# Kernel optimization log

Hardware: AMD Instinct MI355X
Metric: run time of the kernel (lower is better)

## Reference

```python
import jax, jax.numpy as jnp
import numpy as np

_DIMS = [15, 30, 60, 90, 120, 90, 60, 30, 15, 10, 5, 1]


def setup_inputs() -> dict:
    key = jax.random.key(0)
    keys = jax.random.split(key, 1 + 2 * 11)
    inp = {"x": jax.random.normal(keys[0], (524288, 15), dtype=jnp.float32)}
    for i in range(11):
        fan_in, fan_out = _DIMS[i], _DIMS[i + 1]
        bound = 1.0 / np.sqrt(fan_in)
        inp[f"W{i+1}"] = jax.random.uniform(keys[1 + 2 * i], (fan_out, fan_in), minval=-bound, maxval=bound, dtype=jnp.float32)
        inp[f"b{i+1}"] = jax.random.uniform(keys[2 + 2 * i], (fan_out,), minval=-bound, maxval=bound, dtype=jnp.float32)
    return inp


def reference(x, W1, b1, W2, b2, W3, b3, W4, b4, W5, b5, W6, b6, W7, b7, W8, b8, W9, b9, W10, b10, W11, b11):
    Ws = [W1, W2, W3, W4, W5, W6, W7, W8, W9, W10, W11]
    bs = [b1, b2, b3, b4, b5, b6, b7, b8, b9, b10, b11]
    h = x
    # 10 Linear+ReLU layers, funnel 15->30->60->90->120->90->60->30->15->10->5
    for W, b in zip(Ws[:-1], bs[:-1]):
        h = jax.nn.relu(h @ W.T + b)
    # final Linear 5->1 + sigmoid
    return jax.nn.sigmoid(h @ Ws[-1].T + bs[-1])
```

## Files before the change

kernel.cpp:

```cpp
#include <hip/hip_runtime.h>
#include <math.h>


using bf16x8 = __attribute__((ext_vector_type(8))) short;
using f32x4  = __attribute__((ext_vector_type(4))) float;
using u16x8  = __attribute__((ext_vector_type(8))) unsigned short;
using u32x2  = __attribute__((ext_vector_type(2))) unsigned;
typedef __bf16 bf16x2_t __attribute__((ext_vector_type(2)));

namespace {
constexpr int NL = 11;
constexpr int IN_[NL]   = {15, 30, 60, 90, 120, 90, 60, 30, 15, 10, 5};
constexpr int OUT_[NL]  = {30, 60, 90, 120, 90, 60, 30, 15, 10, 5, 1};
constexpr int KP_[NL]   = {32, 32, 64, 96, 128, 96, 64, 32, 32, 32, 32};
constexpr int NP_[NL]   = {32, 64, 96, 128, 96, 64, 32, 16, 16, 16, 16};
constexpr int WOFF_[NL] = {0, 1024, 3072, 9216, 21504, 33792, 39936, 41984, 42496, 43008, 43520};
constexpr int WTOT      = 44032;
constexpr int ACT_OFF   = WTOT;
constexpr int WAVES     = 8;
constexpr int ROWS_PER_BLOCK = WAVES * 32;
constexpr int ARENA     = 4096;
constexpr int LDS_BYTES = (WTOT + WAVES * ARENA) * 2;
}

__device__ __forceinline__ unsigned short f2bf(float f) {
    unsigned u = __float_as_uint(f);
    u += 0x7fffu + ((u >> 16) & 1u);
    return (unsigned short)(u >> 16);
}

__device__ __forceinline__ unsigned pk2(float a, float b) {
#if __has_builtin(__builtin_amdgcn_cvt_pk_bf16_f32)
    return __builtin_bit_cast(unsigned, __builtin_amdgcn_cvt_pk_bf16_f32(a, b));
#else
    bf16x2_t c;
    c[0] = (__bf16)a;
    c[1] = (__bf16)b;
    return __builtin_bit_cast(unsigned, c);
#endif
}

template <int L>
__device__ __forceinline__ void stage_w(const float* __restrict__ W,
                                        const float* __restrict__ B,
                                        short* wlds, int tid) {
    constexpr int KP = KP_[L], NP = NP_[L], INl = IN_[L], OUTl = OUT_[L];
    constexpr int NKT = KP / 32;
    for (int idx = tid; idx < NP * KP; idx += 512) {
        const int f    = idx >> 9;
        const int t    = idx & 511;
        const int quad = t >> 7;
        const int colc = (t >> 3) & 15;
        const int j    = t & 7;
        const int mt   = f / NKT;
        const int kt   = f - mt * NKT;
        const int m    = mt * 16 + colc;
        const int k    = kt * 32 + quad * 8 + j;
        float v = 0.f;
        if (m < OUTl) {
            if (k < INl) v = W[m * INl + k];
            else if (k == INl) v = B[m];
            else if (k == INl + 1) {
                float hf = __builtin_bit_cast(float, (unsigned)f2bf(B[m]) << 16);
                v = B[m] - hf;
            }
        } else if (m == OUTl || m == OUTl + 1) {
            if (k == INl) v = 1.f;
        }
        wlds[WOFF_[L] + idx] = (short)f2bf(v);
    }
}

template <int L>
__device__ __forceinline__ void layer_fwd(const short* __restrict__ wlds,
                                          short* buf, int col, int quad) {
    constexpr int KP   = KP_[L];
    constexpr int NP   = NP_[L];
    constexpr int NKT  = KP / 32;
    constexpr int NMT  = NP / 16;
    constexpr int KPN  = KP_[L + 1];
    constexpr int NKTN = KPN / 32;
    const short* wl = wlds + WOFF_[L];
    const int fo = quad * 128 + col * 8;

    f32x4 acc[NMT][2];
#pragma unroll
    for (int mt = 0; mt < NMT; ++mt)
#pragma unroll
        for (int b = 0; b < 2; ++b)
            acc[mt][b] = f32x4{0.f, 0.f, 0.f, 0.f};

#pragma unroll
    for (int kt = 0; kt < NKT; ++kt) {
        bf16x8 b0 = *(const bf16x8*)(buf + kt * 512 + fo);
        bf16x8 b1 = *(const bf16x8*)(buf + (NKT + kt) * 512 + fo);
#pragma unroll
        for (int mt = 0; mt < NMT; ++mt) {
            bf16x8 af = *(const bf16x8*)(wl + (mt * NKT + kt) * 512 + fo);
            acc[mt][0] = __builtin_amdgcn_mfma_f32_16x16x32_bf16(af, b0, acc[mt][0], 0, 0, 0);
            acc[mt][1] = __builtin_amdgcn_mfma_f32_16x16x32_bf16(af, b1, acc[mt][1], 0, 0, 0);
        }
    }
#pragma unroll
    for (int mt = 0; mt < NMT; ++mt) {
        const int wbase = (mt >> 1) * 512 + ((mt & 1) * 2 + (quad >> 1)) * 128 + col * 8 + (quad & 1) * 4;
#pragma unroll
        for (int b = 0; b < 2; ++b) {
            u32x2 o;
            o[0] = pk2(fmaxf(acc[mt][b][0], 0.f), fmaxf(acc[mt][b][1], 0.f));
            o[1] = pk2(fmaxf(acc[mt][b][2], 0.f), fmaxf(acc[mt][b][3], 0.f));
            *(u32x2*)(buf + b * NKTN * 512 + wbase) = o;
        }
    }
    if constexpr (NP < KPN) {
        u16x8 z = {0, 0, 0, 0, 0, 0, 0, 0};
        if ((quad & 1) == 0) z[0] = (unsigned short)0x3F80;
        *(u16x8*)(buf + (quad >> 1) * NKTN * 512 + (2 + (quad & 1)) * 128 + col * 8) = z;
    }
}

__device__ __forceinline__ void layer_one(bf16x8 af, short* buf, int col, int quad) {
    const int fo = quad * 128 + col * 8;
    bf16x8 b0 = *(const bf16x8*)(buf + fo);
    bf16x8 b1 = *(const bf16x8*)(buf + 512 + fo);
    f32x4 a0 = f32x4{0.f, 0.f, 0.f, 0.f};
    f32x4 a1 = f32x4{0.f, 0.f, 0.f, 0.f};
    a0 = __builtin_amdgcn_mfma_f32_16x16x32_bf16(af, b0, a0, 0, 0, 0);
    a1 = __builtin_amdgcn_mfma_f32_16x16x32_bf16(af, b1, a1, 0, 0, 0);
    const int wbase = (quad >> 1) * 128 + col * 8 + (quad & 1) * 4;
    u32x2 o0, o1;
    o0[0] = pk2(fmaxf(a0[0], 0.f), fmaxf(a0[1], 0.f));
    o0[1] = pk2(fmaxf(a0[2], 0.f), fmaxf(a0[3], 0.f));
    o1[0] = pk2(fmaxf(a1[0], 0.f), fmaxf(a1[1], 0.f));
    o1[1] = pk2(fmaxf(a1[2], 0.f), fmaxf(a1[3], 0.f));
    *(u32x2*)(buf + wbase) = o0;
    *(u32x2*)(buf + 512 + wbase) = o1;
    u16x8 z = {0, 0, 0, 0, 0, 0, 0, 0};
    if ((quad & 1) == 0) z[0] = (unsigned short)0x3F80;
    *(u16x8*)(buf + (quad >> 1) * 512 + (2 + (quad & 1)) * 128 + col * 8) = z;
}

__device__ __forceinline__ float4 ld4(const float* p) {
    float4 t;
    __builtin_memcpy(&t, p, 16);
    return t;
}

__device__ __forceinline__ void fetch_x(const float* __restrict__ x, int row0,
                                        int col, int quad, float4& a0, float4& a1) {
    const float* r0 = x + (long)(row0 + col) * 15;
    const float* r1 = x + (long)(row0 + 16 + col) * 15;
    if (quad < 3) {
        a0 = ld4(r0 + quad * 4);
        a1 = ld4(r1 + quad * 4);
    } else {
        float4 t0 = ld4(r0 + 11), t1 = ld4(r1 + 11);
        a0 = make_float4(t0.y, t0.z, t0.w, 1.f);
        a1 = make_float4(t1.y, t1.z, t1.w, 1.f);
    }
}

__device__ __forceinline__ void stage_x(short* buf, float4 a0, float4 a1,
                                        int col, int quad) {
    const int off = (quad >> 1) * 128 + col * 8 + (quad & 1) * 4;
    u32x2 o0, o1;
    o0[0] = pk2(a0.x, a0.y); o0[1] = pk2(a0.z, a0.w);
    o1[0] = pk2(a1.x, a1.y); o1[1] = pk2(a1.z, a1.w);
    *(u32x2*)(buf + off) = o0;
    *(u32x2*)(buf + 512 + off) = o1;
    u16x8 z = {0, 0, 0, 0, 0, 0, 0, 0};
    if ((quad & 1) == 0) z[0] = (unsigned short)0x3F80;
    *(u16x8*)(buf + (quad >> 1) * 512 + (2 + (quad & 1)) * 128 + col * 8) = z;
}

extern "C" __global__ void __launch_bounds__(512, 2)
mlp_fused(const float* __restrict__ x,
          const float* __restrict__ W0,  const float* __restrict__ B0,
          const float* __restrict__ W1,  const float* __restrict__ B1,
          const float* __restrict__ W2,  const float* __restrict__ B2,
          const float* __restrict__ W3,  const float* __restrict__ B3,
          const float* __restrict__ W4,  const float* __restrict__ B4,
          const float* __restrict__ W5,  const float* __restrict__ B5,
          const float* __restrict__ W6,  const float* __restrict__ B6,
          const float* __restrict__ W7,  const float* __restrict__ B7,
          const float* __restrict__ W8,  const float* __restrict__ B8,
          const float* __restrict__ W9,  const float* __restrict__ B9,
          const float* __restrict__ W10, const float* __restrict__ B10,
          float* __restrict__ out, int nchunks) {
    extern __shared__ short smem[];
    short* wlds = smem;
    short* act  = smem + ACT_OFF;

    const int tid = threadIdx.x;

    stage_w<0>(W0, B0, wlds, tid);
    stage_w<1>(W1, B1, wlds, tid);
    stage_w<2>(W2, B2, wlds, tid);
    stage_w<3>(W3, B3, wlds, tid);
    stage_w<4>(W4, B4, wlds, tid);
    stage_w<5>(W5, B5, wlds, tid);
    stage_w<6>(W6, B6, wlds, tid);
    stage_w<7>(W7, B7, wlds, tid);
    stage_w<8>(W8, B8, wlds, tid);
    stage_w<9>(W9, B9, wlds, tid);
    stage_w<10>(W10, B10, wlds, tid);
    __syncthreads();

    const int wave = tid >> 6;
    const int lane = tid & 63;
    const int col  = lane & 15;
    const int quad = lane >> 4;
    short* buf = act + wave * ARENA;
    const int fo = quad * 128 + col * 8;

    const bf16x8 w7  = *(const bf16x8*)(wlds + WOFF_[7]  + fo);
    const bf16x8 w8  = *(const bf16x8*)(wlds + WOFF_[8]  + fo);
    const bf16x8 w9  = *(const bf16x8*)(wlds + WOFF_[9]  + fo);
    const bf16x8 w10 = *(const bf16x8*)(wlds + WOFF_[10] + fo);

    int chunk = blockIdx.x;
    float4 xa, xb;
    if (chunk < nchunks)
        fetch_x(x, chunk * ROWS_PER_BLOCK + wave * 32, col, quad, xa, xb);

    for (; chunk < nchunks; chunk += gridDim.x) {
        const int row0 = chunk * ROWS_PER_BLOCK + wave * 32;
        stage_x(buf, xa, xb, col, quad);

        const int nxt = chunk + gridDim.x;
        if (nxt < nchunks)
            fetch_x(x, nxt * ROWS_PER_BLOCK + wave * 32, col, quad, xa, xb);

        layer_fwd<0>(wlds, buf, col, quad);
        layer_fwd<1>(wlds, buf, col, quad);
        layer_fwd<2>(wlds, buf, col, quad);
        layer_fwd<3>(wlds, buf, col, quad);
        layer_fwd<4>(wlds, buf, col, quad);
        layer_fwd<5>(wlds, buf, col, quad);
        layer_fwd<6>(wlds, buf, col, quad);
        layer_one(w7, buf, col, quad);
        layer_one(w8, buf, col, quad);
        layer_one(w9, buf, col, quad);

        {
            bf16x8 b0 = *(const bf16x8*)(buf + fo);
            bf16x8 b1 = *(const bf16x8*)(buf + 512 + fo);
            f32x4 a0 = f32x4{0.f, 0.f, 0.f, 0.f};
            f32x4 a1 = f32x4{0.f, 0.f, 0.f, 0.f};
            a0 = __builtin_amdgcn_mfma_f32_16x16x32_bf16(w10, b0, a0, 0, 0, 0);
            a1 = __builtin_amdgcn_mfma_f32_16x16x32_bf16(w10, b1, a1, 0, 0, 0);
            if (quad == 0) {
                out[row0 + col]      = 1.f / (1.f + __expf(-a0[0]));
                out[row0 + 16 + col] = 1.f / (1.f + __expf(-a1[0]));
            }
        }
    }
}

extern "C" void kernel_launch(void* const* d_in, const int* in_sizes, int n_in,
                              void* d_out, int out_size, void* d_ws, size_t ws_size,
                              hipStream_t stream) {
    (void)n_in; (void)d_ws; (void)ws_size; (void)out_size;
    const float* x = (const float*)d_in[0];
    const float* W[11];
    const float* B[11];
    for (int i = 0; i < 11; ++i) {
        W[i] = (const float*)d_in[1 + 2 * i];
        B[i] = (const float*)d_in[2 + 2 * i];
    }
    const int nrows   = in_sizes[0] / 15;
    const int nchunks = nrows / ROWS_PER_BLOCK;

    hipFuncSetAttribute((const void*)mlp_fused,
                        hipFuncAttributeMaxDynamicSharedMemorySize, LDS_BYTES);

    mlp_fused<<<dim3(256), dim3(512), LDS_BYTES, stream>>>(
        x,
        W[0], B[0], W[1], B[1], W[2], B[2], W[3], B[3], W[4], B[4],
        W[5], B[5], W[6], B[6], W[7], B[7], W[8], B[8], W[9], B[9],
        W[10], B[10],
        (float*)d_out, nchunks);
}
```

Measured before the change: 196.8 us.

## Process 64 rows per wave and keep middle-layer activations in registers via shuffles

Each wave now handles 64 rows (four 16-row tiles) instead of 32, so every weight fragment read from LDS feeds four MFMAs instead of two. For layers 2–4 the activations stay in registers: the MFMA output layout is turned into the next layer's B-operand layout with cross-lane shuffles instead of an LDS round trip. The cost is much higher register pressure under launch_bounds(512,2), with possible spills, plus extra shuffle instructions. Per-wave arena usage also grows, and it needs to still fit within ARENA.

```diff
diff --git a/kernel.cpp b/kernel.cpp
--- a/kernel.cpp
+++ b/kernel.cpp
@@ -6,6 +6,7 @@
 using f32x4  = __attribute__((ext_vector_type(4))) float;
 using u16x8  = __attribute__((ext_vector_type(8))) unsigned short;
 using u32x2  = __attribute__((ext_vector_type(2))) unsigned;
+using u32x4  = __attribute__((ext_vector_type(4))) unsigned;
 typedef __bf16 bf16x2_t __attribute__((ext_vector_type(2)));
 
 namespace {
@@ -16,9 +17,8 @@
 constexpr int NP_[NL]   = {32, 64, 96, 128, 96, 64, 32, 16, 16, 16, 16};
 constexpr int WOFF_[NL] = {0, 1024, 3072, 9216, 21504, 33792, 39936, 41984, 42496, 43008, 43520};
 constexpr int WTOT      = 44032;
-constexpr int ACT_OFF   = WTOT;
 constexpr int WAVES     = 8;
-constexpr int ROWS_PER_BLOCK = WAVES * 32;
+constexpr int ROWS_PER_BLOCK = 512;
 constexpr int ARENA     = 4096;
 constexpr int LDS_BYTES = (WTOT + WAVES * ARENA) * 2;
 }
@@ -38,6 +38,30 @@
     c[1] = (__bf16)b;
     return __builtin_bit_cast(unsigned, c);
 #endif
+}
+
+__device__ __forceinline__ u32x2 packrelu(f32x4 a) {
+    u32x2 p;
+    p[0] = pk2(fmaxf(a[0], 0.f), fmaxf(a[1], 0.f));
+    p[1] = pk2(fmaxf(a[2], 0.f), fmaxf(a[3], 0.f));
+    return p;
+}
+
+__device__ __forceinline__ bf16x8 xform(u32x2 pa, u32x2 pb, bool sel, int sA, int sB) {
+    int a0 = __shfl((int)pa[0], sA);
+    int b0 = __shfl((int)pb[0], sA);
+    int a1 = __shfl((int)pa[1], sA);
+    int b1 = __shfl((int)pb[1], sA);
+    int a2 = __shfl((int)pa[0], sB);
+    int b2 = __shfl((int)pb[0], sB);
+    int a3 = __shfl((int)pa[1], sB);
+    int b3 = __shfl((int)pb[1], sB);
+    u32x4 r;
+    r[0] = (unsigned)(sel ? b0 : a0);
+    r[1] = (unsigned)(sel ? b1 : a1);
+    r[2] = (unsigned)(sel ? b2 : a2);
+    r[3] = (unsigned)(sel ? b3 : a3);
+    return __builtin_bit_cast(bf16x8, r);
 }
 
 template <int L>
@@ -72,72 +96,116 @@
 }
 
 template <int L>
-__device__ __forceinline__ void layer_fwd(const short* __restrict__ wlds,
-                                          short* buf, int col, int quad) {
-    constexpr int KP   = KP_[L];
-    constexpr int NP   = NP_[L];
-    constexpr int NKT  = KP / 32;
-    constexpr int NMT  = NP / 16;
-    constexpr int KPN  = KP_[L + 1];
-    constexpr int NKTN = KPN / 32;
+__device__ __forceinline__ void layer_lds(const short* __restrict__ wlds,
+                                          short* buf, int col, int quad, int fo) {
+    constexpr int NKT  = KP_[L] / 32;
+    constexpr int NMT  = NP_[L] / 16;
+    constexpr int NKTN = KP_[L + 1] / 32;
     const short* wl = wlds + WOFF_[L];
-    const int fo = quad * 128 + col * 8;
-
-    f32x4 acc[NMT][2];
+    bf16x8 bin[4][NKT];
+#pragma unroll
+    for (int t = 0; t < 4; ++t)
+#pragma unroll
+        for (int kt = 0; kt < NKT; ++kt)
+            bin[t][kt] = *(const bf16x8*)(buf + (t * NKT + kt) * 512 + fo);
+    f32x4 acc[NMT][4];
 #pragma unroll
     for (int mt = 0; mt < NMT; ++mt)
 #pragma unroll
-        for (int b = 0; b < 2; ++b)
-            acc[mt][b] = f32x4{0.f, 0.f, 0.f, 0.f};
-
-#pragma unroll
-    for (int kt = 0; kt < NKT; ++kt) {
-        bf16x8 b0 = *(const bf16x8*)(buf + kt * 512 + fo);
-        bf16x8 b1 = *(const bf16x8*)(buf + (NKT + kt) * 512 + fo);
+        for (int t = 0; t < 4; ++t)
+            acc[mt][t] = f32x4{0.f, 0.f, 0.f, 0.f};
+#pragma unroll
+    for (int kt = 0; kt < NKT; ++kt)
 #pragma unroll
         for (int mt = 0; mt < NMT; ++mt) {
             bf16x8 af = *(const bf16x8*)(wl + (mt * NKT + kt) * 512 + fo);
-            acc[mt][0] = __builtin_amdgcn_mfma_f32_16x16x32_bf16(af, b0, acc[mt][0], 0, 0, 0);
-            acc[mt][1] = __builtin_amdgcn_mfma_f32_16x16x32_bf16(af, b1, acc[mt][1], 0, 0, 0);
-        }
-    }
+#pragma unroll
+            for (int t = 0; t < 4; ++t)
+                acc[mt][t] = __builtin_amdgcn_mfma_f32_16x16x32_bf16(af, bin[t][kt], acc[mt][t], 0, 0, 0);
+        }
 #pragma unroll
     for (int mt = 0; mt < NMT; ++mt) {
         const int wbase = (mt >> 1) * 512 + ((mt & 1) * 2 + (quad >> 1)) * 128 + col * 8 + (quad & 1) * 4;
 #pragma unroll
-        for (int b = 0; b < 2; ++b) {
-            u32x2 o;
-            o[0] = pk2(fmaxf(acc[mt][b][0], 0.f), fmaxf(acc[mt][b][1], 0.f));
-            o[1] = pk2(fmaxf(acc[mt][b][2], 0.f), fmaxf(acc[mt][b][3], 0.f));
-            *(u32x2*)(buf + b * NKTN * 512 + wbase) = o;
-        }
-    }
-    if constexpr (NP < KPN) {
-        u16x8 z = {0, 0, 0, 0, 0, 0, 0, 0};
-        if ((quad & 1) == 0) z[0] = (unsigned short)0x3F80;
-        *(u16x8*)(buf + (quad >> 1) * NKTN * 512 + (2 + (quad & 1)) * 128 + col * 8) = z;
-    }
-}
-
-__device__ __forceinline__ void layer_one(bf16x8 af, short* buf, int col, int quad) {
-    const int fo = quad * 128 + col * 8;
-    bf16x8 b0 = *(const bf16x8*)(buf + fo);
-    bf16x8 b1 = *(const bf16x8*)(buf + 512 + fo);
-    f32x4 a0 = f32x4{0.f, 0.f, 0.f, 0.f};
-    f32x4 a1 = f32x4{0.f, 0.f, 0.f, 0.f};
-    a0 = __builtin_amdgcn_mfma_f32_16x16x32_bf16(af, b0, a0, 0, 0, 0);
-    a1 = __builtin_amdgcn_mfma_f32_16x16x32_bf16(af, b1, a1, 0, 0, 0);
+        for (int t = 0; t < 4; ++t)
+            *(u32x2*)(buf + t * NKTN * 512 + wbase) = packrelu(acc[mt][t]);
+    }
+}
+
+template <int L>
+__device__ __forceinline__ void reg_pair(const short* __restrict__ wlds, int g,
+                                         const bf16x8 (&bin)[KP_[L] / 32][4],
+                                         bf16x8 (&bout)[4],
+                                         bool sel, int sA, int sB, int fo) {
+    constexpr int NKT = KP_[L] / 32;
+    const short* wl = wlds + WOFF_[L];
+    f32x4 acc0[4], acc1[4];
+#pragma unroll
+    for (int t = 0; t < 4; ++t) {
+        acc0[t] = f32x4{0.f, 0.f, 0.f, 0.f};
+        acc1[t] = f32x4{0.f, 0.f, 0.f, 0.f};
+    }
+#pragma unroll
+    for (int kt = 0; kt < NKT; ++kt) {
+        bf16x8 a0 = *(const bf16x8*)(wl + ((2 * g) * NKT + kt) * 512 + fo);
+        bf16x8 a1 = *(const bf16x8*)(wl + ((2 * g + 1) * NKT + kt) * 512 + fo);
+#pragma unroll
+        for (int t = 0; t < 4; ++t) {
+            acc0[t] = __builtin_amdgcn_mfma_f32_16x16x32_bf16(a0, bin[kt][t], acc0[t], 0, 0, 0);
+            acc1[t] = __builtin_amdgcn_mfma_f32_16x16x32_bf16(a1, bin[kt][t], acc1[t], 0, 0, 0);
+        }
+    }
+#pragma unroll
+    for (int t = 0; t < 4; ++t)
+        bout[t] = xform(packrelu(acc0[t]), packrelu(acc1[t]), sel, sA, sB);
+}
+
+__device__ __forceinline__ void l5_to_lds(const short* __restrict__ wlds,
+                                          const bf16x8 (&h5)[3][4],
+                                          short* buf, int col, int quad, int fo) {
+    const short* wl = wlds + WOFF_[5];
+    f32x4 acc[4][4];
+#pragma unroll
+    for (int mt = 0; mt < 4; ++mt)
+#pragma unroll
+        for (int t = 0; t < 4; ++t)
+            acc[mt][t] = f32x4{0.f, 0.f, 0.f, 0.f};
+#pragma unroll
+    for (int kt = 0; kt < 3; ++kt)
+#pragma unroll
+        for (int mt = 0; mt < 4; ++mt) {
+            bf16x8 af = *(const bf16x8*)(wl + (mt * 3 + kt) * 512 + fo);
+#pragma unroll
+            for (int t = 0; t < 4; ++t)
+                acc[mt][t] = __builtin_amdgcn_mfma_f32_16x16x32_bf16(af, h5[kt][t], acc[mt][t], 0, 0, 0);
+        }
+#pragma unroll
+    for (int mt = 0; mt < 4; ++mt) {
+        const int wbase = (mt >> 1) * 512 + ((mt & 1) * 2 + (quad >> 1)) * 128 + col * 8 + (quad & 1) * 4;
+#pragma unroll
+        for (int t = 0; t < 4; ++t)
+            *(u32x2*)(buf + t * 2 * 512 + wbase) = packrelu(acc[mt][t]);
+    }
+}
+
+__device__ __forceinline__ void layer_one4(bf16x8 af, short* buf, int col, int quad, int fo) {
+    bf16x8 b[4];
+#pragma unroll
+    for (int t = 0; t < 4; ++t) b[t] = *(const bf16x8*)(buf + t * 512 + fo);
+    f32x4 a[4];
+#pragma unroll
+    for (int t = 0; t < 4; ++t) {
+        a[t] = f32x4{0.f, 0.f, 0.f, 0.f};
+        a[t] = __builtin_amdgcn_mfma_f32_16x16x32_bf16(af, b[t], a[t], 0, 0, 0);
+    }
     const int wbase = (quad >> 1) * 128 + col * 8 + (quad & 1) * 4;
-    u32x2 o0, o1;
-    o0[0] = pk2(fmaxf(a0[0], 0.f), fmaxf(a0[1], 0.f));
-    o0[1] = pk2(fmaxf(a0[2], 0.f), fmaxf(a0[3], 0.f));
-    o1[0] = pk2(fmaxf(a1[0], 0.f), fmaxf(a1[1], 0.f));
-    o1[1] = pk2(fmaxf(a1[2], 0.f), fmaxf(a1[3], 0.f));
-    *(u32x2*)(buf + wbase) = o0;
-    *(u32x2*)(buf + 512 + wbase) = o1;
+#pragma unroll
+    for (int t = 0; t < 4; ++t)
+        *(u32x2*)(buf + t * 512 + wbase) = packrelu(a[t]);
     u16x8 z = {0, 0, 0, 0, 0, 0, 0, 0};
-    if ((quad & 1) == 0) z[0] = (unsigned short)0x3F80;
+    if (!(quad & 1)) z[0] = (unsigned short)0x3F80;
     *(u16x8*)(buf + (quad >> 1) * 512 + (2 + (quad & 1)) * 128 + col * 8) = z;
+    *(u16x8*)(buf + ((quad >> 1) + 2) * 512 + (2 + (quad & 1)) * 128 + col * 8) = z;
 }
 
 __device__ __forceinline__ float4 ld4(const float* p) {
@@ -146,31 +214,34 @@
     return t;
 }
 
-__device__ __forceinline__ void fetch_x(const float* __restrict__ x, int row0,
-                                        int col, int quad, float4& a0, float4& a1) {
-    const float* r0 = x + (long)(row0 + col) * 15;
-    const float* r1 = x + (long)(row0 + 16 + col) * 15;
-    if (quad < 3) {
-        a0 = ld4(r0 + quad * 4);
-        a1 = ld4(r1 + quad * 4);
-    } else {
-        float4 t0 = ld4(r0 + 11), t1 = ld4(r1 + 11);
-        a0 = make_float4(t0.y, t0.z, t0.w, 1.f);
-        a1 = make_float4(t1.y, t1.z, t1.w, 1.f);
-    }
-}
-
-__device__ __forceinline__ void stage_x(short* buf, float4 a0, float4 a1,
-                                        int col, int quad) {
+__device__ __forceinline__ void fetch_x4(const float* __restrict__ x, int row0,
+                                         int col, int quad, float4 (&xv)[4]) {
+#pragma unroll
+    for (int t = 0; t < 4; ++t) {
+        const float* xr = x + (long)(row0 + t * 16 + col) * 15;
+        if (quad < 3) {
+            xv[t] = ld4(xr + quad * 4);
+        } else {
+            float4 u = ld4(xr + 11);
+            xv[t] = make_float4(u.y, u.z, u.w, 1.f);
+        }
+    }
+}
+
+__device__ __forceinline__ void stage_x4(short* buf, const float4 (&xv)[4],
+                                         int col, int quad) {
     const int off = (quad >> 1) * 128 + col * 8 + (quad & 1) * 4;
-    u32x2 o0, o1;
-    o0[0] = pk2(a0.x, a0.y); o0[1] = pk2(a0.z, a0.w);
-    o1[0] = pk2(a1.x, a1.y); o1[1] = pk2(a1.z, a1.w);
-    *(u32x2*)(buf + off) = o0;
-    *(u32x2*)(buf + 512 + off) = o1;
+#pragma unroll
+    for (int t = 0; t < 4; ++t) {
+        u32x2 o;
+        o[0] = pk2(xv[t].x, xv[t].y);
+        o[1] = pk2(xv[t].z, xv[t].w);
+        *(u32x2*)(buf + t * 512 + off) = o;
+    }
     u16x8 z = {0, 0, 0, 0, 0, 0, 0, 0};
-    if ((quad & 1) == 0) z[0] = (unsigned short)0x3F80;
+    if (!(quad & 1)) z[0] = (unsigned short)0x3F80;
     *(u16x8*)(buf + (quad >> 1) * 512 + (2 + (quad & 1)) * 128 + col * 8) = z;
+    *(u16x8*)(buf + ((quad >> 1) + 2) * 512 + (2 + (quad & 1)) * 128 + col * 8) = z;
 }
 
 extern "C" __global__ void __launch_bounds__(512, 2)
@@ -187,9 +258,9 @@
           const float* __restrict__ W9,  const float* __restrict__ B9,
           const float* __restrict__ W10, const float* __restrict__ B10,
           float* __restrict__ out, int nchunks) {
-    extern __shared__ short smem[];
+    extern __shared__ __align__(16) short smem[];
     short* wlds = smem;
-    short* act  = smem + ACT_OFF;
+    short* act  = smem + WTOT;
 
     const int tid = threadIdx.x;
 
@@ -212,6 +283,9 @@
     const int quad = lane >> 4;
     short* buf = act + wave * ARENA;
     const int fo = quad * 128 + col * 8;
+    const bool sel = quad >= 2;
+    const int sA = col + 16 * (2 * (quad & 1));
+    const int sB = sA + 16;
 
     const bf16x8 w7  = *(const bf16x8*)(wlds + WOFF_[7]  + fo);
     const bf16x8 w8  = *(const bf16x8*)(wlds + WOFF_[8]  + fo);
@@ -219,39 +293,62 @@
     const bf16x8 w10 = *(const bf16x8*)(wlds + WOFF_[10] + fo);
 
     int chunk = blockIdx.x;
-    float4 xa, xb;
+    float4 xv[4];
     if (chunk < nchunks)
-        fetch_x(x, chunk * ROWS_PER_BLOCK + wave * 32, col, quad, xa, xb);
+        fetch_x4(x, chunk * ROWS_PER_BLOCK + wave * 64, col, quad, xv);
 
     for (; chunk < nchunks; chunk += gridDim.x) {
-        const int row0 = chunk * ROWS_PER_BLOCK + wave * 32;
-        stage_x(buf, xa, xb, col, quad);
+        const int row0 = chunk * ROWS_PER_BLOCK + wave * 64;
+        stage_x4(buf, xv, col, quad);
 
         const int nxt = chunk + gridDim.x;
         if (nxt < nchunks)
-            fetch_x(x, nxt * ROWS_PER_BLOCK + wave * 32, col, quad, xa, xb);
-
-        layer_fwd<0>(wlds, buf, col, quad);
-        layer_fwd<1>(wlds, buf, col, quad);
-        layer_fwd<2>(wlds, buf, col, quad);
-        layer_fwd<3>(wlds, buf, col, quad);
-        layer_fwd<4>(wlds, buf, col, quad);
-        layer_fwd<5>(wlds, buf, col, quad);
-        layer_fwd<6>(wlds, buf, col, quad);
-        layer_one(w7, buf, col, quad);
-        layer_one(w8, buf, col, quad);
-        layer_one(w9, buf, col, quad);
+            fetch_x4(x, nxt * ROWS_PER_BLOCK + wave * 64, col, quad, xv);
+
+        layer_lds<0>(wlds, buf, col, quad, fo);
+        layer_lds<1>(wlds, buf, col, quad, fo);
+
+        bf16x8 h2[2][4];
+#pragma unroll
+        for (int kt = 0; kt < 2; ++kt)
+#pragma unroll
+            for (int t = 0; t < 4; ++t)
+                h2[kt][t] = *(const bf16x8*)(buf + (t * 2 + kt) * 512 + fo);
+
+        bf16x8 h3[3][4];
+#pragma unroll
+        for (int g = 0; g < 3; ++g)
+            reg_pair<2>(wlds, g, h2, h3[g], sel, sA, sB, fo);
+
+        bf16x8 h4[4][4];
+#pragma unroll
+        for (int g = 0; g < 4; ++g)
+            reg_pair<3>(wlds, g, h3, h4[g], sel, sA, sB, fo);
+
+        bf16x8 h5[3][4];
+#pragma unroll
+        for (int g = 0; g < 3; ++g)
+            reg_pair<4>(wlds, g, h4, h5[g], sel, sA, sB, fo);
+
+        l5_to_lds(wlds, h5, buf, col, quad, fo);
+
+        layer_lds<6>(wlds, buf, col, quad, fo);
+        layer_one4(w7, buf, col, quad, fo);
+        layer_one4(w8, buf, col, quad, fo);
+        layer_one4(w9, buf, col, quad, fo);
 
         {
-            bf16x8 b0 = *(const bf16x8*)(buf + fo);
-            bf16x8 b1 = *(const bf16x8*)(buf + 512 + fo);
-            f32x4 a0 = f32x4{0.f, 0.f, 0.f, 0.f};
-            f32x4 a1 = f32x4{0.f, 0.f, 0.f, 0.f};
-            a0 = __builtin_amdgcn_mfma_f32_16x16x32_bf16(w10, b0, a0, 0, 0, 0);
-            a1 = __builtin_amdgcn_mfma_f32_16x16x32_bf16(w10, b1, a1, 0, 0, 0);
+            f32x4 a[4];
+#pragma unroll
+            for (int t = 0; t < 4; ++t) {
+                bf16x8 b = *(const bf16x8*)(buf + t * 512 + fo);
+                a[t] = f32x4{0.f, 0.f, 0.f, 0.f};
+                a[t] = __builtin_amdgcn_mfma_f32_16x16x32_bf16(w10, b, a[t], 0, 0, 0);
+            }
             if (quad == 0) {
-                out[row0 + col]      = 1.f / (1.f + __expf(-a0[0]));
-                out[row0 + 16 + col] = 1.f / (1.f + __expf(-a1[0]));
+#pragma unroll
+                for (int t = 0; t < 4; ++t)
+                    out[row0 + t * 16 + col] = 1.f / (1.f + __expf(-a[t][0]));
             }
         }
     }
```

Result: slower. 201.9 us (+2.6%).
